# Kernel tuning notes

Measured on AMD Instinct MI355X. Metric: run time of the kernel, lower is better.

The kernel has to match this reference:

```python
import jax, jax.numpy as jnp
import numpy as np

B, T, D, H = 128, 1024, 1024, 1024


def setup_inputs() -> dict:
    key = jax.random.key(0)
    ks = jax.random.split(key, 13)
    s_in = (6.0 / (D + H)) ** 0.5   # xavier_uniform bound for [D,H]
    s_hh = (6.0 / (H + H)) ** 0.5   # xavier_uniform bound for [H,H]
    def wu(k, shape, s):
        return jax.random.uniform(k, shape, jnp.float32, -s, s)
    inp = {
        'x': jax.random.normal(ks[0], (B, T, D), jnp.float32),
        'W_ii': wu(ks[1], (D, H), s_in),
        'W_if': wu(ks[2], (D, H), s_in),
        'W_ig': wu(ks[3], (D, H), s_in),
        'W_io': wu(ks[4], (D, H), s_in),
        'W_hi': wu(ks[5], (H, H), s_hh),
        'W_hf': wu(ks[6], (H, H), s_hh),
        'W_hg': wu(ks[7], (H, H), s_hh),
        'W_ho': wu(ks[8], (H, H), s_hh),
        'b_i': jnp.zeros((H,), jnp.float32),
        'b_f': jnp.zeros((H,), jnp.float32),
        'b_g': jnp.zeros((H,), jnp.float32),
        'b_o': jnp.zeros((H,), jnp.float32),
    }
    return inp


def reference(x, W_ii, W_if, W_ig, W_io, W_hi, W_hf, W_hg, W_ho, b_i, b_f, b_g, b_o):
    b, t, d = x.shape
    h = W_ii.shape[1]
    # Fuse the 4 gate projections into single GEMMs (same math as 8 separate mm's).
    Wi = jnp.concatenate([W_ii, W_if, W_ig, W_io], axis=1)  # [D, 4H]
    Wh = jnp.concatenate([W_hi, W_hf, W_hg, W_ho], axis=1)  # [H, 4H]
    bias = jnp.concatenate([b_i, b_f, b_g, b_o])            # [4H]
    # Precompute all input projections in one big GEMM: [T, B, 4H]
    x_proj = jnp.einsum('btd,dg->tbg', x, Wi) + bias

    def step(carry, xp):
        h_t, c_t = carry
        gates = xp + h_t @ Wh                      # [B, 4H]
        i_t = jax.nn.sigmoid(gates[:, 0 * h:1 * h])
        f_t = jax.nn.sigmoid(gates[:, 1 * h:2 * h])
        g_t = jnp.tanh(gates[:, 2 * h:3 * h])
        o_t = jax.nn.sigmoid(gates[:, 3 * h:4 * h])
        c_t = f_t * c_t + i_t * g_t
        h_t = o_t * jnp.tanh(c_t)
        return (h_t, c_t), None

    init = (jnp.zeros((b, h), x.dtype), jnp.zeros((b, h), x.dtype))
    (h_t, c_t), _ = jax.lax.scan(step, init, x_proj)
    return h_t, c_t
```

## Files before the change

kernel.cpp:

```cpp
#include <hip/hip_runtime.h>
#include <hip/hip_bf16.h>


typedef __attribute__((ext_vector_type(8))) short short8;
typedef __attribute__((ext_vector_type(4))) float floatx4;
typedef __attribute__((ext_vector_type(4))) unsigned int uint4v;
typedef unsigned long long u64;
typedef unsigned short u16;

#define NB 128
#define NTT 1024

__device__ __attribute__((aligned(256))) u16 g_xpack[(size_t)NTT * NB * 1024];
__device__ __attribute__((aligned(256))) u16 g_wpack[2][4194304];
__device__ __attribute__((aligned(256))) u16 g_hall[NTT][NB * 1024];
__device__ __attribute__((aligned(256))) unsigned g_cnt[4 * 64];

__device__ __forceinline__ u16 f2bf(float f) {
  unsigned u = __float_as_uint(f);
  u += 0x7FFFu + ((u >> 16) & 1u);
  return (u16)(u >> 16);
}

__global__ void pack_w(const float* __restrict__ Wii, const float* __restrict__ Wif,
                       const float* __restrict__ Wig, const float* __restrict__ Wio,
                       const float* __restrict__ Whi, const float* __restrict__ Whf,
                       const float* __restrict__ Whg, const float* __restrict__ Who) {
  int wid = (blockIdx.x << 2) | (threadIdx.x >> 6);
  int lane = threadIdx.x & 63;
  int mat = wid >> 13;
  int rem = wid & 8191;
  int cb = rem >> 7;
  int ks = (rem >> 2) & 31;
  int nt = rem & 3;
  int n = lane & 15, quad = lane >> 4;
  const float *Wlo, *Whi2;
  if (mat == 0) { Wlo = (nt & 1) ? Wig : Wii; Whi2 = (nt & 1) ? Wio : Wif; }
  else          { Wlo = (nt & 1) ? Whg : Whi; Whi2 = (nt & 1) ? Who : Whf; }
  const float* src = (n < 8) ? Wlo : Whi2;
  int col = (cb << 4) + ((nt >> 1) << 3) + (n & 7);
  int k0 = (ks << 5) + (quad << 3);
  u16 tmp[8];
#pragma unroll
  for (int j = 0; j < 8; ++j) tmp[j] = f2bf(src[(size_t)(k0 + j) * 1024 + col]);
  *(uint4v*)&g_wpack[mat][((size_t)((cb * 32 + ks) * 4 + nt) << 9) + lane * 8] = *(uint4v*)tmp;
}

__global__ void pack_x(const float* __restrict__ x) {
  int pair = threadIdx.x >> 7;
  int kt = (threadIdx.x & 127) << 3;
  int bt = (blockIdx.x << 1) | pair;
  int b = bt >> 10, t = bt & 1023;
  const float* src = x + ((size_t)b * 1024 + t) * 1024 + kt;
  u16 tmp[8];
#pragma unroll
  for (int j = 0; j < 8; ++j) tmp[j] = f2bf(src[j]);
  *(uint4v*)&g_xpack[((size_t)t * NB + b) * 1024 + kt] = *(uint4v*)tmp;
  if (bt < 128) {
    size_t base = ((size_t)bt << 10) + ((size_t)(threadIdx.x & 127) << 3);
    uint4v z = {0u, 0u, 0u, 0u};
    *(uint4v*)&g_hall[0][base] = z;
  }
  if (bt == 0 && threadIdx.x == 0) {
#pragma unroll
    for (int r = 0; r < 4; ++r) g_cnt[r << 6] = 0u;
  }
}

__global__ __launch_bounds__(256, 1) void lstm_main(
    const float* __restrict__ bi, const float* __restrict__ bf,
    const float* __restrict__ bg, const float* __restrict__ bo,
    float* __restrict__ out) {
  __shared__ u16 whlds[65536];
  __shared__ float xbuf[2][32][68];
  __shared__ unsigned ld_epoch;

  const int tid = threadIdx.x;
  const int wave = tid >> 6, lane = tid & 63;
  const int wm = wave >> 1, wn = wave & 1;
  const int wg = blockIdx.x;
  const int xcd = wg & 7;
  const int rb = xcd & 3;
  const int cb = ((xcd >> 2) << 5) | (wg >> 3);
  const int rowbase = rb << 5;
  const int n = lane & 15, quad = lane >> 4;

  if (tid == 0) ld_epoch = 0u;

  {
    const u16* src = &g_wpack[1][(size_t)cb << 16];
#pragma unroll 4
    for (int i = 0; i < 32; ++i) {
      int off = ((i << 8) + tid) << 3;
      *(uint4v*)&whlds[off] = *(const uint4v*)&src[off];
    }
  }

  const int colb = (cb << 4) | (wn << 3) | (n & 7);
  const float bias0 = (n < 8) ? bi[colb] : bf[colb];
  const float bias1 = (n < 8) ? bg[colb] : bo[colb];

  float creg[2][4];
#pragma unroll
  for (int m = 0; m < 2; ++m)
#pragma unroll
    for (int r = 0; r < 4; ++r) creg[m][r] = 0.f;

  const u16* wip = &g_wpack[0][(size_t)cb << 16];
  unsigned* cnt = &g_cnt[rb << 6];

  __syncthreads();

  for (int tt = 0; tt <= 1024; ++tt) {
    __syncthreads();
    if (tid == 128 && tt >= 2)
      __hip_atomic_fetch_add(cnt, 1u, __ATOMIC_RELAXED, __HIP_MEMORY_SCOPE_AGENT);

    if (wm == 0) {
      if (tt < 1024) {
        const u16* xp = &g_xpack[((size_t)tt * NB + rowbase) << 10];
        floatx4 acc[2][2];
#pragma unroll
        for (int m = 0; m < 2; ++m) {
          acc[m][0] = floatx4{bias0, bias0, bias0, bias0};
          acc[m][1] = floatx4{bias1, bias1, bias1, bias1};
        }
        short8 A[2][2][4], Bv[2][2][4];
#pragma unroll
        for (int j = 0; j < 4; ++j) {
#pragma unroll
          for (int m = 0; m < 2; ++m)
            A[0][m][j] = *(const short8*)&xp[(((m << 4) | n) << 10) + (j << 5) + (quad << 3)];
#pragma unroll
          for (int q = 0; q < 2; ++q)
            Bv[0][q][j] = *(const short8*)&wip[(((j << 2) | (wn << 1) | q) << 9) + (lane << 3)];
        }
#pragma unroll
        for (int c = 0; c < 8; ++c) {
          int cur = c & 1, nxt = cur ^ 1;
          if (c < 7) {
#pragma unroll
            for (int j = 0; j < 4; ++j) {
              int ks = ((c + 1) << 2) | j;
#pragma unroll
              for (int m = 0; m < 2; ++m)
                A[nxt][m][j] =
                    *(const short8*)&xp[(((m << 4) | n) << 10) + (ks << 5) + (quad << 3)];
#pragma unroll
              for (int q = 0; q < 2; ++q)
                Bv[nxt][q][j] =
                    *(const short8*)&wip[(((ks << 2) | (wn << 1) | q) << 9) + (lane << 3)];
            }
          }
#pragma unroll
          for (int j = 0; j < 4; ++j)
#pragma unroll
            for (int m = 0; m < 2; ++m)
#pragma unroll
              for (int q = 0; q < 2; ++q)
                acc[m][q] = __builtin_amdgcn_mfma_f32_16x16x32_bf16(
                    A[cur][m][j], Bv[cur][q][j], acc[m][q], 0, 0, 0);
        }
        int p = tt & 1;
#pragma unroll
        for (int m = 0; m < 2; ++m)
#pragma unroll
          for (int q = 0; q < 2; ++q)
#pragma unroll
            for (int r = 0; r < 4; ++r)
              xbuf[p][(m << 4) + (quad << 2) + r][(((wn << 1) | q) << 4) | n] = acc[m][q][r];
      }
    } else if (tt >= 1) {
      const int t = tt - 1;
      if (t > 0) {
        const unsigned target = (unsigned)t << 6;
        if (wave == 2) {
          int guard = 0;
          for (;;) {
            unsigned cur = 0;
            if (lane == 0)
              cur = __hip_atomic_load(cnt, __ATOMIC_RELAXED, __HIP_MEMORY_SCOPE_AGENT);
            cur = __builtin_amdgcn_readfirstlane(cur);
            if (cur >= target) break;
            __builtin_amdgcn_s_sleep(2);
            if (++guard > (1 << 20)) break;
          }
          if (lane == 0) *(volatile unsigned*)&ld_epoch = (unsigned)t;
        } else {
          int guard = 0;
          while (*(volatile unsigned*)&ld_epoch < (unsigned)t) {
            __builtin_amdgcn_s_sleep(2);
            if (++guard > (1 << 20)) break;
          }
        }
      }
      asm volatile("" ::: "memory");

      floatx4 acc[2][2];
      int p = t & 1;
#pragma unroll
      for (int m = 0; m < 2; ++m)
#pragma unroll
        for (int q = 0; q < 2; ++q)
#pragma unroll
          for (int r = 0; r < 4; ++r)
            acc[m][q][r] = xbuf[p][(m << 4) + (quad << 2) + r][(((wn << 1) | q) << 4) | n];

      const u16* hp = &g_hall[t][rowbase << 10];
      short8 A[2][2][8];
#pragma unroll
      for (int j = 0; j < 8; ++j)
#pragma unroll
        for (int m = 0; m < 2; ++m)
          A[0][m][j] = *(const short8*)&hp[(((m << 4) | n) << 10) + (j << 5) + (quad << 3)];
#pragma unroll
      for (int c = 0; c < 4; ++c) {
        int cur = c & 1, nxt = cur ^ 1;
        if (c < 3) {
#pragma unroll
          for (int j = 0; j < 8; ++j) {
            int ks = ((c + 1) << 3) | j;
#pragma unroll
            for (int m = 0; m < 2; ++m)
              A[nxt][m][j] =
                  *(const short8*)&hp[(((m << 4) | n) << 10) + (ks << 5) + (quad << 3)];
          }
        }
#pragma unroll
        for (int j = 0; j < 8; ++j) {
          int ks = (c << 3) | j;
          short8 b0 = *(const short8*)&whlds[(((ks << 2) | (wn << 1)) << 9) + (lane << 3)];
          short8 b1 = *(const short8*)&whlds[(((ks << 2) | (wn << 1) | 1) << 9) + (lane << 3)];
#pragma unroll
          for (int m = 0; m < 2; ++m) {
            acc[m][0] = __builtin_amdgcn_mfma_f32_16x16x32_bf16(A[cur][m][j], b0, acc[m][0], 0, 0, 0);
            acc[m][1] = __builtin_amdgcn_mfma_f32_16x16x32_bf16(A[cur][m][j], b1, acc[m][1], 0, 0, 0);
          }
        }
      }
      const int colbase = (cb << 4) | (wn << 3);
      u16* hw = (t < 1023) ? &g_hall[t + 1][0] : (u16*)0;
#pragma unroll
      for (int m = 0; m < 2; ++m)
#pragma unroll
        for (int r = 0; r < 4; ++r) {
          float v0 = acc[m][0][r], v1 = acc[m][1][r];
          float q0 = __shfl_xor(v0, 8, 64);
          float q1 = __shfl_xor(v1, 8, 64);
          bool lo = (n < 8);
          float ipre = lo ? v0 : q0;
          float fpre = lo ? q0 : v0;
          float gpre = lo ? v1 : q1;
          float opre = lo ? q1 : v1;
          float iv = 1.f / (1.f + __expf(-ipre));
          float fv = 1.f / (1.f + __expf(-fpre));
          float eg = __expf(2.f * gpre);
          float gv = 1.f - 2.f / (eg + 1.f);
          float ov = 1.f / (1.f + __expf(-opre));
          float cn = fv * creg[m][r] + iv * gv;
          creg[m][r] = cn;
          float ec = __expf(2.f * cn);
          float tc = 1.f - 2.f / (ec + 1.f);
          float hn = ov * tc;
          int row = rowbase + (m << 4) + (quad << 2) + r;
          if (t < 1023) {
            unsigned hv = (unsigned)f2bf(hn);
            unsigned u01 = (hv & 0xFFFFu) | (((unsigned)__shfl_xor((int)hv, 1, 64)) << 16);
            unsigned u23 = (unsigned)__shfl_xor((int)u01, 2, 64);
            if (lo && (n & 3) == 0) {
              u64 pk = (u64)u01 | ((u64)u23 << 32);
              __hip_atomic_store((u64*)&hw[(row << 10) + colbase + n], pk,
                                 __ATOMIC_RELAXED, __HIP_MEMORY_SCOPE_AGENT);
            }
          } else if (lo) {
            int col = colbase | n;
            out[(row << 10) + col] = hn;
            out[131072 + (row << 10) + col] = cn;
          }
        }
      asm volatile("" ::: "memory");
      __builtin_amdgcn_s_waitcnt(0);
    }
  }
}

extern "C" void kernel_launch(void* const* d_in, const int* in_sizes, int n_in,
                              void* d_out, int out_size, void* d_ws, size_t ws_size,
                              hipStream_t stream) {
  const float* x   = (const float*)d_in[0];
  const float* Wii = (const float*)d_in[1];
  const float* Wif = (const float*)d_in[2];
  const float* Wig = (const float*)d_in[3];
  const float* Wio = (const float*)d_in[4];
  const float* Whi = (const float*)d_in[5];
  const float* Whf = (const float*)d_in[6];
  const float* Whg = (const float*)d_in[7];
  const float* Who = (const float*)d_in[8];
  const float* bi  = (const float*)d_in[9];
  const float* bf_ = (const float*)d_in[10];
  const float* bg  = (const float*)d_in[11];
  const float* bo  = (const float*)d_in[12];
  float* out = (float*)d_out;

  pack_w<<<4096, 256, 0, stream>>>(Wii, Wif, Wig, Wio, Whi, Whf, Whg, Who);
  pack_x<<<65536, 256, 0, stream>>>(x);
  lstm_main<<<256, 256, 0, stream>>>(bi, bf_, bg, bo, out);
}
```

Before: 19.85 ms.

## Precompute input projection in a prologue and use per-block flags for recurrence sync

Moves the x·W_i projection out of the per-timestep loop into a prologue: each block first loads W_i into LDS, computes projections for all 1024 timesteps, and stores them as fp16 in a global buffer. The recurrent loop then has all four waves doing the h·W_h GEMM, each on 16 rows, and reads the precomputed projection directly. The single counter incremented by atomic add is replaced by per-block flags that a whole wave polls and checks with __all. This removes the per-step input GEMM from the serial critical path, at the cost of a large extra global buffer, fp16 rounding of the projections, and a serialized prologue that no longer overlaps with the recurrence.

Result: faster. 18.57 ms (-6.4%).

```diff
diff --git a/kernel.cpp b/kernel.cpp
--- a/kernel.cpp
+++ b/kernel.cpp
@@ -5,6 +5,7 @@
 typedef __attribute__((ext_vector_type(8))) short short8;
 typedef __attribute__((ext_vector_type(4))) float floatx4;
 typedef __attribute__((ext_vector_type(4))) unsigned int uint4v;
+typedef __attribute__((ext_vector_type(4))) _Float16 half4;
 typedef unsigned long long u64;
 typedef unsigned short u16;
 
@@ -14,7 +15,8 @@
 __device__ __attribute__((aligned(256))) u16 g_xpack[(size_t)NTT * NB * 1024];
 __device__ __attribute__((aligned(256))) u16 g_wpack[2][4194304];
 __device__ __attribute__((aligned(256))) u16 g_hall[NTT][NB * 1024];
-__device__ __attribute__((aligned(256))) unsigned g_cnt[4 * 64];
+__device__ __attribute__((aligned(256))) u16 g_xproj[(size_t)NTT * 256 * 2048];
+__device__ __attribute__((aligned(256))) unsigned g_flags[256];
 
 __device__ __forceinline__ u16 f2bf(float f) {
   unsigned u = __float_as_uint(f);
@@ -61,10 +63,7 @@
     uint4v z = {0u, 0u, 0u, 0u};
     *(uint4v*)&g_hall[0][base] = z;
   }
-  if (bt == 0 && threadIdx.x == 0) {
-#pragma unroll
-    for (int r = 0; r < 4; ++r) g_cnt[r << 6] = 0u;
-  }
+  if (blockIdx.x == 0) g_flags[threadIdx.x] = 0u;
 }
 
 __global__ __launch_bounds__(256, 1) void lstm_main(
@@ -72,12 +71,9 @@
     const float* __restrict__ bg, const float* __restrict__ bo,
     float* __restrict__ out) {
   __shared__ u16 whlds[65536];
-  __shared__ float xbuf[2][32][68];
-  __shared__ unsigned ld_epoch;
 
   const int tid = threadIdx.x;
   const int wave = tid >> 6, lane = tid & 63;
-  const int wm = wave >> 1, wn = wave & 1;
   const int wg = blockIdx.x;
   const int xcd = wg & 7;
   const int rb = xcd & 3;
@@ -85,7 +81,74 @@
   const int rowbase = rb << 5;
   const int n = lane & 15, quad = lane >> 4;
 
-  if (tid == 0) ld_epoch = 0u;
+  {
+    const u16* src = &g_wpack[0][(size_t)cb << 16];
+#pragma unroll 4
+    for (int i = 0; i < 32; ++i) {
+      int off = ((i << 8) + tid) << 3;
+      *(uint4v*)&whlds[off] = *(const uint4v*)&src[off];
+    }
+  }
+  __syncthreads();
+
+  {
+    const int pwn = wave & 1, tpar = wave >> 1;
+    const int pcolb = (cb << 4) | (pwn << 3) | (n & 7);
+    const float pb0 = (n < 8) ? bi[pcolb] : bf[pcolb];
+    const float pb1 = (n < 8) ? bg[pcolb] : bo[pcolb];
+    for (int t = tpar; t < NTT; t += 2) {
+      const u16* xp = &g_xpack[((size_t)t * NB + rowbase) << 10];
+      floatx4 acc[2][2];
+#pragma unroll
+      for (int m = 0; m < 2; ++m) {
+        acc[m][0] = floatx4{pb0, pb0, pb0, pb0};
+        acc[m][1] = floatx4{pb1, pb1, pb1, pb1};
+      }
+      short8 A[2][2][4];
+#pragma unroll
+      for (int j = 0; j < 4; ++j)
+#pragma unroll
+        for (int m = 0; m < 2; ++m)
+          A[0][m][j] = *(const short8*)&xp[(((m << 4) | n) << 10) + (j << 5) + (quad << 3)];
+#pragma unroll
+      for (int c = 0; c < 8; ++c) {
+        int cur = c & 1, nxt = cur ^ 1;
+        if (c < 7) {
+#pragma unroll
+          for (int j = 0; j < 4; ++j) {
+            int ks = ((c + 1) << 2) | j;
+#pragma unroll
+            for (int m = 0; m < 2; ++m)
+              A[nxt][m][j] =
+                  *(const short8*)&xp[(((m << 4) | n) << 10) + (ks << 5) + (quad << 3)];
+          }
+        }
+#pragma unroll
+        for (int j = 0; j < 4; ++j) {
+          int ks = (c << 2) | j;
+          short8 b0 = *(const short8*)&whlds[(((ks << 2) | (pwn << 1)) << 9) + (lane << 3)];
+          short8 b1 = *(const short8*)&whlds[(((ks << 2) | (pwn << 1) | 1) << 9) + (lane << 3)];
+#pragma unroll
+          for (int m = 0; m < 2; ++m) {
+            acc[m][0] = __builtin_amdgcn_mfma_f32_16x16x32_bf16(A[cur][m][j], b0, acc[m][0], 0, 0, 0);
+            acc[m][1] = __builtin_amdgcn_mfma_f32_16x16x32_bf16(A[cur][m][j], b1, acc[m][1], 0, 0, 0);
+          }
+        }
+      }
+      u16* dst = &g_xproj[(((size_t)t << 8) + (rb << 6) + cb) << 11];
+#pragma unroll
+      for (int m = 0; m < 2; ++m)
+#pragma unroll
+        for (int q = 0; q < 2; ++q) {
+          int t8 = (((m << 1) | pwn) << 1) | q;
+          half4 hv;
+#pragma unroll
+          for (int r = 0; r < 4; ++r) hv[r] = (_Float16)acc[m][q][r];
+          *(half4*)&dst[(t8 << 8) + (quad << 6) + (n << 2)] = hv;
+        }
+    }
+  }
+  __syncthreads();
 
   {
     const u16* src = &g_wpack[1][(size_t)cb << 16];
@@ -95,192 +158,101 @@
       *(uint4v*)&whlds[off] = *(const uint4v*)&src[off];
     }
   }
-
-  const int colb = (cb << 4) | (wn << 3) | (n & 7);
-  const float bias0 = (n < 8) ? bi[colb] : bf[colb];
-  const float bias1 = (n < 8) ? bg[colb] : bo[colb];
-
-  float creg[2][4];
-#pragma unroll
-  for (int m = 0; m < 2; ++m)
-#pragma unroll
-    for (int r = 0; r < 4; ++r) creg[m][r] = 0.f;
-
-  const u16* wip = &g_wpack[0][(size_t)cb << 16];
-  unsigned* cnt = &g_cnt[rb << 6];
-
   __syncthreads();
 
-  for (int tt = 0; tt <= 1024; ++tt) {
+  const int cwm = wave >> 1, cwn = wave & 1;
+  const int colbase = (cb << 4) | (cwn << 3);
+  float creg[4] = {0.f, 0.f, 0.f, 0.f};
+  unsigned* myflag = &g_flags[(rb << 6) | cb];
+  unsigned* rbflags = &g_flags[rb << 6];
+
+  for (int t = 0; t < NTT; ++t) {
+    const u16* xsrc = &g_xproj[(((size_t)t << 8) + (rb << 6) + cb) << 11];
+    half4 xh0 = *(const half4*)&xsrc[((((cwm << 1) | cwn) << 1) << 8) + (quad << 6) + (n << 2)];
+    half4 xh1 =
+        *(const half4*)&xsrc[(((((cwm << 1) | cwn) << 1) | 1) << 8) + (quad << 6) + (n << 2)];
+
+    if (t > 0) {
+      int guard = 0;
+      for (;;) {
+        unsigned v = __hip_atomic_load(&rbflags[lane], __ATOMIC_RELAXED, __HIP_MEMORY_SCOPE_AGENT);
+        if (__all((int)(v >= (unsigned)t))) break;
+        __builtin_amdgcn_s_sleep(2);
+        if (++guard > (1 << 20)) break;
+      }
+    }
+    asm volatile("" ::: "memory");
+
+    const u16* hp = &g_hall[t][(rowbase + (cwm << 4)) << 10];
+    floatx4 acc0, acc1;
+#pragma unroll
+    for (int r = 0; r < 4; ++r) { acc0[r] = (float)xh0[r]; acc1[r] = (float)xh1[r]; }
+    short8 A[2][8];
+#pragma unroll
+    for (int j = 0; j < 8; ++j)
+      A[0][j] = *(const short8*)&hp[(n << 10) + (j << 5) + (quad << 3)];
+#pragma unroll
+    for (int c = 0; c < 4; ++c) {
+      int cur = c & 1, nxt = cur ^ 1;
+      if (c < 3) {
+#pragma unroll
+        for (int j = 0; j < 8; ++j) {
+          int ks = ((c + 1) << 3) | j;
+          A[nxt][j] = *(const short8*)&hp[(n << 10) + (ks << 5) + (quad << 3)];
+        }
+      }
+#pragma unroll
+      for (int j = 0; j < 8; ++j) {
+        int ks = (c << 3) | j;
+        short8 b0 = *(const short8*)&whlds[(((ks << 2) | (cwn << 1)) << 9) + (lane << 3)];
+        short8 b1 = *(const short8*)&whlds[(((ks << 2) | (cwn << 1) | 1) << 9) + (lane << 3)];
+        acc0 = __builtin_amdgcn_mfma_f32_16x16x32_bf16(A[cur][j], b0, acc0, 0, 0, 0);
+        acc1 = __builtin_amdgcn_mfma_f32_16x16x32_bf16(A[cur][j], b1, acc1, 0, 0, 0);
+      }
+    }
+
+    u16* hw = (t < 1023) ? &g_hall[t + 1][0] : (u16*)0;
+#pragma unroll
+    for (int r = 0; r < 4; ++r) {
+      float v0 = acc0[r], v1 = acc1[r];
+      float q0 = __shfl_xor(v0, 8, 64);
+      float q1 = __shfl_xor(v1, 8, 64);
+      bool lo = (n < 8);
+      float ipre = lo ? v0 : q0;
+      float fpre = lo ? q0 : v0;
+      float gpre = lo ? v1 : q1;
+      float opre = lo ? q1 : v1;
+      float iv = 1.f / (1.f + __expf(-ipre));
+      float fv = 1.f / (1.f + __expf(-fpre));
+      float eg = __expf(2.f * gpre);
+      float gv = 1.f - 2.f / (eg + 1.f);
+      float ov = 1.f / (1.f + __expf(-opre));
+      float cn = fv * creg[r] + iv * gv;
+      creg[r] = cn;
+      float ec = __expf(2.f * cn);
+      float tc = 1.f - 2.f / (ec + 1.f);
+      float hn = ov * tc;
+      int row = rowbase + (cwm << 4) + (quad << 2) + r;
+      if (t < 1023) {
+        unsigned hv = (unsigned)f2bf(hn);
+        unsigned u01 = (hv & 0xFFFFu) | (((unsigned)__shfl_xor((int)hv, 1, 64)) << 16);
+        unsigned u23 = (unsigned)__shfl_xor((int)u01, 2, 64);
+        if (lo && (n & 3) == 0) {
+          u64 pk = (u64)u01 | ((u64)u23 << 32);
+          __hip_atomic_store((u64*)&hw[(row << 10) + colbase + n], pk,
+                             __ATOMIC_RELAXED, __HIP_MEMORY_SCOPE_AGENT);
+        }
+      } else if (lo) {
+        int col = colbase | n;
+        out[(row << 10) + col] = hn;
+        out[131072 + (row << 10) + col] = cn;
+      }
+    }
+    asm volatile("" ::: "memory");
+    __builtin_amdgcn_s_waitcnt(0);
     __syncthreads();
-    if (tid == 128 && tt >= 2)
-      __hip_atomic_fetch_add(cnt, 1u, __ATOMIC_RELAXED, __HIP_MEMORY_SCOPE_AGENT);
-
-    if (wm == 0) {
-      if (tt < 1024) {
-        const u16* xp = &g_xpack[((size_t)tt * NB + rowbase) << 10];
-        floatx4 acc[2][2];
-#pragma unroll
-        for (int m = 0; m < 2; ++m) {
-          acc[m][0] = floatx4{bias0, bias0, bias0, bias0};
-          acc[m][1] = floatx4{bias1, bias1, bias1, bias1};
-        }
-        short8 A[2][2][4], Bv[2][2][4];
-#pragma unroll
-        for (int j = 0; j < 4; ++j) {
-#pragma unroll
-          for (int m = 0; m < 2; ++m)
-            A[0][m][j] = *(const short8*)&xp[(((m << 4) | n) << 10) + (j << 5) + (quad << 3)];
-#pragma unroll
-          for (int q = 0; q < 2; ++q)
-            Bv[0][q][j] = *(const short8*)&wip[(((j << 2) | (wn << 1) | q) << 9) + (lane << 3)];
-        }
-#pragma unroll
-        for (int c = 0; c < 8; ++c) {
-          int cur = c & 1, nxt = cur ^ 1;
-          if (c < 7) {
-#pragma unroll
-            for (int j = 0; j < 4; ++j) {
-              int ks = ((c + 1) << 2) | j;
-#pragma unroll
-              for (int m = 0; m < 2; ++m)
-                A[nxt][m][j] =
-                    *(const short8*)&xp[(((m << 4) | n) << 10) + (ks << 5) + (quad << 3)];
-#pragma unroll
-              for (int q = 0; q < 2; ++q)
-                Bv[nxt][q][j] =
-                    *(const short8*)&wip[(((ks << 2) | (wn << 1) | q) << 9) + (lane << 3)];
-            }
-          }
-#pragma unroll
-          for (int j = 0; j < 4; ++j)
-#pragma unroll
-            for (int m = 0; m < 2; ++m)
-#pragma unroll
-              for (int q = 0; q < 2; ++q)
-                acc[m][q] = __builtin_amdgcn_mfma_f32_16x16x32_bf16(
-                    A[cur][m][j], Bv[cur][q][j], acc[m][q], 0, 0, 0);
-        }
-        int p = tt & 1;
-#pragma unroll
-        for (int m = 0; m < 2; ++m)
-#pragma unroll
-          for (int q = 0; q < 2; ++q)
-#pragma unroll
-            for (int r = 0; r < 4; ++r)
-              xbuf[p][(m << 4) + (quad << 2) + r][(((wn << 1) | q) << 4) | n] = acc[m][q][r];
-      }
-    } else if (tt >= 1) {
-      const int t = tt - 1;
-      if (t > 0) {
-        const unsigned target = (unsigned)t << 6;
-        if (wave == 2) {
-          int guard = 0;
-          for (;;) {
-            unsigned cur = 0;
-            if (lane == 0)
-              cur = __hip_atomic_load(cnt, __ATOMIC_RELAXED, __HIP_MEMORY_SCOPE_AGENT);
-            cur = __builtin_amdgcn_readfirstlane(cur);
-            if (cur >= target) break;
-            __builtin_amdgcn_s_sleep(2);
-            if (++guard > (1 << 20)) break;
-          }
-          if (lane == 0) *(volatile unsigned*)&ld_epoch = (unsigned)t;
-        } else {
-          int guard = 0;
-          while (*(volatile unsigned*)&ld_epoch < (unsigned)t) {
-            __builtin_amdgcn_s_sleep(2);
-            if (++guard > (1 << 20)) break;
-          }
-        }
-      }
-      asm volatile("" ::: "memory");
-
-      floatx4 acc[2][2];
-      int p = t & 1;
-#pragma unroll
-      for (int m = 0; m < 2; ++m)
-#pragma unroll
-        for (int q = 0; q < 2; ++q)
-#pragma unroll
-          for (int r = 0; r < 4; ++r)
-            acc[m][q][r] = xbuf[p][(m << 4) + (quad << 2) + r][(((wn << 1) | q) << 4) | n];
-
-      const u16* hp = &g_hall[t][rowbase << 10];
-      short8 A[2][2][8];
-#pragma unroll
-      for (int j = 0; j < 8; ++j)
-#pragma unroll
-        for (int m = 0; m < 2; ++m)
-          A[0][m][j] = *(const short8*)&hp[(((m << 4) | n) << 10) + (j << 5) + (quad << 3)];
-#pragma unroll
-      for (int c = 0; c < 4; ++c) {
-        int cur = c & 1, nxt = cur ^ 1;
-        if (c < 3) {
-#pragma unroll
-          for (int j = 0; j < 8; ++j) {
-            int ks = ((c + 1) << 3) | j;
-#pragma unroll
-            for (int m = 0; m < 2; ++m)
-              A[nxt][m][j] =
-                  *(const short8*)&hp[(((m << 4) | n) << 10) + (ks << 5) + (quad << 3)];
-          }
-        }
-#pragma unroll
-        for (int j = 0; j < 8; ++j) {
-          int ks = (c << 3) | j;
-          short8 b0 = *(const short8*)&whlds[(((ks << 2) | (wn << 1)) << 9) + (lane << 3)];
-          short8 b1 = *(const short8*)&whlds[(((ks << 2) | (wn << 1) | 1) << 9) + (lane << 3)];
-#pragma unroll
-          for (int m = 0; m < 2; ++m) {
-            acc[m][0] = __builtin_amdgcn_mfma_f32_16x16x32_bf16(A[cur][m][j], b0, acc[m][0], 0, 0, 0);
-            acc[m][1] = __builtin_amdgcn_mfma_f32_16x16x32_bf16(A[cur][m][j], b1, acc[m][1], 0, 0, 0);
-          }
-        }
-      }
-      const int colbase = (cb << 4) | (wn << 3);
-      u16* hw = (t < 1023) ? &g_hall[t + 1][0] : (u16*)0;
-#pragma unroll
-      for (int m = 0; m < 2; ++m)
-#pragma unroll
-        for (int r = 0; r < 4; ++r) {
-          float v0 = acc[m][0][r], v1 = acc[m][1][r];
-          float q0 = __shfl_xor(v0, 8, 64);
-          float q1 = __shfl_xor(v1, 8, 64);
-          bool lo = (n < 8);
-          float ipre = lo ? v0 : q0;
-          float fpre = lo ? q0 : v0;
-          float gpre = lo ? v1 : q1;
-          float opre = lo ? q1 : v1;
-          float iv = 1.f / (1.f + __expf(-ipre));
-          float fv = 1.f / (1.f + __expf(-fpre));
-          float eg = __expf(2.f * gpre);
-          float gv = 1.f - 2.f / (eg + 1.f);
-          float ov = 1.f / (1.f + __expf(-opre));
-          float cn = fv * creg[m][r] + iv * gv;
-          creg[m][r] = cn;
-          float ec = __expf(2.f * cn);
-          float tc = 1.f - 2.f / (ec + 1.f);
-          float hn = ov * tc;
-          int row = rowbase + (m << 4) + (quad << 2) + r;
-          if (t < 1023) {
-            unsigned hv = (unsigned)f2bf(hn);
-            unsigned u01 = (hv & 0xFFFFu) | (((unsigned)__shfl_xor((int)hv, 1, 64)) << 16);
-            unsigned u23 = (unsigned)__shfl_xor((int)u01, 2, 64);
-            if (lo && (n & 3) == 0) {
-              u64 pk = (u64)u01 | ((u64)u23 << 32);
-              __hip_atomic_store((u64*)&hw[(row << 10) + colbase + n], pk,
-                                 __ATOMIC_RELAXED, __HIP_MEMORY_SCOPE_AGENT);
-            }
-          } else if (lo) {
-            int col = colbase | n;
-            out[(row << 10) + col] = hn;
-            out[131072 + (row << 10) + col] = cn;
-          }
-        }
-      asm volatile("" ::: "memory");
-      __builtin_amdgcn_s_waitcnt(0);
-    }
+    if (tid == 0 && t < 1023)
+      __hip_atomic_store(myflag, (unsigned)(t + 1), __ATOMIC_RELAXED, __HIP_MEMORY_SCOPE_AGENT);
   }
 }
 
```
